# Optimization experiments

Hardware: AMD Instinct MI355X
Metric: run time of the kernel (lower is better)

Reference implementation:

```python
import jax, jax.numpy as jnp
import numpy as np

IN_C = 128
OUT_C = 128
N_NODES = 50000
N_EDGES = 500000


def setup_inputs() -> dict:
    key = jax.random.key(0)
    ks = jax.random.split(key, 12)
    s = lambda k, shp, fan: jax.random.normal(k, shp, jnp.float32) * (1.0 / np.sqrt(fan))
    return {
        "node_embeddings": jax.random.normal(ks[0], (N_NODES, IN_C), jnp.float32),
        "edge_index": jax.random.randint(ks[1], (2, N_EDGES), 0, N_NODES, jnp.int64),
        # source_proj / target_proj: Linear(in, in)
        "Ws": s(ks[2], (IN_C, IN_C), IN_C), "bs": jnp.zeros((IN_C,), jnp.float32),
        "Wt": s(ks[3], (IN_C, IN_C), IN_C), "bt": jnp.zeros((IN_C,), jnp.float32),
        # attention_mlp: Linear(2in, in) -> ReLU -> Linear(in, 1) -> Sigmoid
        "Wa1": s(ks[4], (2 * IN_C, IN_C), 2 * IN_C), "ba1": jnp.zeros((IN_C,), jnp.float32),
        "Wa2": s(ks[5], (IN_C, 1), IN_C), "ba2": jnp.zeros((1,), jnp.float32),
        # edge_mlp: Linear(2in, 2out) -> GeGLU -> LayerNorm(out)
        "We": s(ks[6], (2 * IN_C, 2 * OUT_C), 2 * IN_C), "be": jnp.zeros((2 * OUT_C,), jnp.float32),
        "gamma": jnp.ones((OUT_C,), jnp.float32), "beta": jnp.zeros((OUT_C,), jnp.float32),
    }


def reference(node_embeddings, edge_index, Ws, bs, Wt, bt, Wa1, ba1, Wa2, ba2, We, be, gamma, beta):
    # gather + dual projection  -> [E, in], [E, in]
    src = node_embeddings[edge_index[0]] @ Ws + bs
    tgt = node_embeddings[edge_index[1]] @ Wt + bt
    edge_features = jnp.concatenate([src, tgt], axis=-1)  # [E, 2*in]
    # sigmoid attention gate  -> [E, 1]
    h = jax.nn.relu(edge_features @ Wa1 + ba1)
    attn = jax.nn.sigmoid(h @ Wa2 + ba2)
    attended = edge_features * attn  # [E, 2*in]
    # edge MLP: Linear -> GeGLU -> LayerNorm
    z = attended @ We + be  # [E, 2*out]
    x, gate = jnp.split(z, 2, axis=-1)
    g = x * jax.nn.gelu(gate, approximate=False)  # [E, out]
    mu = jnp.mean(g, axis=-1, keepdims=True)
    var = jnp.var(g, axis=-1, keepdims=True)
    out = (g - mu) * jax.lax.rsqrt(var + 1e-5) * gamma + beta
    return out
```

## Files before the change

kernel.cpp:

```cpp
#include <hip/hip_runtime.h>
#include <hip/hip_bf16.h>


typedef __bf16 bf16x8 __attribute__((ext_vector_type(8)));
typedef float f32x4 __attribute__((ext_vector_type(4)));

__device__ __forceinline__ unsigned short f2b(float f) {
    unsigned int u = __float_as_uint(f);
    unsigned int r = (u + 0x7fffu + ((u >> 16) & 1u)) >> 16;
    return (unsigned short)r;
}

__device__ __forceinline__ float erf_fast(float x) {
    float ax = __builtin_fabsf(x);
    float t = __fdividef(1.f, fmaf(0.3275911f, ax, 1.f));
    float y = t * fmaf(t, fmaf(t, fmaf(t, fmaf(t, 1.061405429f, -1.453152027f),
                                       1.421413741f), -0.284496736f), 0.254829592f);
    float e = __expf(-ax * ax);
    float r = fmaf(-y, e, 1.f);
    return __builtin_copysignf(r, x);
}

__global__ __launch_bounds__(256) void pack_weights(
    const float* __restrict__ Ws, const float* __restrict__ Wt,
    const float* __restrict__ Wa1, const float* __restrict__ We,
    unsigned short* __restrict__ Wp1, unsigned short* __restrict__ Wp2)
{
    int id = blockIdx.x * 256 + threadIdx.x;
    if (id < 32768) {
        int n = id >> 7, k = id & 127;
        float v = (n < 128) ? Ws[k * 128 + n] : Wt[k * 128 + (n - 128)];
        Wp1[id] = f2b(v);
    }
    if (id < 98304) {
        int n = id >> 8, k = id & 255;
        float v = (n < 128) ? Wa1[k * 128 + n] : We[k * 256 + (n - 128)];
        Wp2[id] = f2b(v);
    }
}

__global__ __launch_bounds__(256) void node_proj(
    const float* __restrict__ emb, const unsigned short* __restrict__ Wp1,
    const float* __restrict__ bs, const float* __restrict__ bt,
    unsigned short* __restrict__ P, int NN)
{
    __shared__ __align__(16) unsigned short SH[64 * 264];
    int t = threadIdx.x;
    int base = blockIdx.x * 64;

#pragma unroll
    for (int i = 0; i < 4; ++i) {
        int c = t + i * 256;
        int row = c >> 4, cp = (c & 15) * 8;
        int node = base + row; if (node >= NN) node = NN - 1;
        const float* sp = emb + (size_t)node * 128 + cp;
        float4 v0 = *(const float4*)sp;
        float4 v1 = *(const float4*)(sp + 4);
        union { uint4 u; unsigned short s[8]; } pk;
        pk.s[0] = f2b(v0.x); pk.s[1] = f2b(v0.y); pk.s[2] = f2b(v0.z); pk.s[3] = f2b(v0.w);
        pk.s[4] = f2b(v1.x); pk.s[5] = f2b(v1.y); pk.s[6] = f2b(v1.z); pk.s[7] = f2b(v1.w);
        *(uint4*)&SH[row * 136 + cp] = pk.u;
    }
    __syncthreads();

    int wv = t >> 6, lane = t & 63, n15 = lane & 15, quad = lane >> 4;
    f32x4 z4 = {0.f, 0.f, 0.f, 0.f};
    f32x4 acc[16];
#pragma unroll
    for (int i = 0; i < 16; ++i) acc[i] = z4;

    const unsigned short* wbase = Wp1 + (size_t)(wv * 16 + n15) * 128 + quad * 8;
    for (int ks = 0; ks < 4; ++ks) {
        bf16x8 a[4];
#pragma unroll
        for (int m = 0; m < 4; ++m)
            a[m] = *(const bf16x8*)&SH[(m * 16 + n15) * 136 + ks * 32 + quad * 8];
#pragma unroll
        for (int k = 0; k < 4; ++k) {
            bf16x8 b = *(const bf16x8*)(wbase + k * 8192 + ks * 32);
#pragma unroll
            for (int m = 0; m < 4; ++m)
                acc[k * 4 + m] = __builtin_amdgcn_mfma_f32_16x16x32_bf16(a[m], b, acc[k * 4 + m], 0, 0, 0);
        }
    }
    __syncthreads();

#pragma unroll
    for (int k = 0; k < 4; ++k) {
        int colk = (wv + 4 * k) * 16 + n15;
        float bias = (colk < 128) ? bs[colk] : bt[colk - 128];
#pragma unroll
        for (int m = 0; m < 4; ++m) {
#pragma unroll
            for (int r = 0; r < 4; ++r)
                SH[(m * 16 + quad * 4 + r) * 264 + colk] = f2b(acc[k * 4 + m][r] + bias);
        }
    }
    __syncthreads();

#pragma unroll
    for (int i = 0; i < 8; ++i) {
        int e = i * 8 + (t >> 5);
        int node = base + e;
        if (node < NN) {
            int c = (t & 31) * 8;
            *(uint4*)(P + (size_t)node * 256 + c) = *(const uint4*)&SH[e * 264 + c];
        }
    }
}

__global__ __launch_bounds__(256, 3) void edge_kernel(
    const int* __restrict__ eidx, const unsigned short* __restrict__ P,
    const unsigned short* __restrict__ Wp2,
    const float* __restrict__ ba1, const float* __restrict__ Wa2,
    const float* __restrict__ ba2, const float* __restrict__ be,
    const float* __restrict__ gamma, const float* __restrict__ beta,
    float* __restrict__ out, int E)
{
    __shared__ unsigned short Alds[64][264];
    __shared__ float attnP[4][64];
    __shared__ float lnP[4][2][64];
    int t = threadIdx.x;
    int base = blockIdx.x * 64;

#pragma unroll
    for (int i = 0; i < 8; ++i) {
        int c = t + i * 256;
        int e = c >> 5, p = c & 31;
        int ge = base + e; if (ge >= E) ge = E - 1;
        int node = (p < 16) ? eidx[ge] : eidx[E + ge];
        *(uint4*)&Alds[e][p * 8] = *(const uint4*)(P + (size_t)node * 256 + p * 8);
    }
    __syncthreads();

    int wv = t >> 6, lane = t & 63, n15 = lane & 15, quad = lane >> 4;
    f32x4 z4 = {0.f, 0.f, 0.f, 0.f};
    const unsigned short* wbase = Wp2 + (size_t)(wv * 16 + n15) * 256 + quad * 8;

    f32x4 acc1[8];
#pragma unroll
    for (int i = 0; i < 8; ++i) acc1[i] = z4;
    for (int ks = 0; ks < 8; ++ks) {
        bf16x8 a[4];
#pragma unroll
        for (int m = 0; m < 4; ++m)
            a[m] = *(const bf16x8*)&Alds[m * 16 + n15][ks * 32 + quad * 8];
#pragma unroll
        for (int n = 0; n < 2; ++n) {
            bf16x8 b = *(const bf16x8*)(wbase + n * 16384 + ks * 32);
#pragma unroll
            for (int m = 0; m < 4; ++m)
                acc1[n * 4 + m] = __builtin_amdgcn_mfma_f32_16x16x32_bf16(a[m], b, acc1[n * 4 + m], 0, 0, 0);
        }
    }

    float ba2s = ba2[0];
    float ba1v[2], wa2v[2];
#pragma unroll
    for (int n = 0; n < 2; ++n) {
        int col = (wv + 4 * n) * 16 + n15;
        ba1v[n] = ba1[col]; wa2v[n] = Wa2[col];
    }
#pragma unroll
    for (int m = 0; m < 4; ++m) {
#pragma unroll
        for (int r = 0; r < 4; ++r) {
            float v = fmaxf(acc1[m][r] + ba1v[0], 0.f) * wa2v[0]
                    + fmaxf(acc1[4 + m][r] + ba1v[1], 0.f) * wa2v[1];
            v += __shfl_xor(v, 1); v += __shfl_xor(v, 2);
            v += __shfl_xor(v, 4); v += __shfl_xor(v, 8);
            if (n15 == m * 4 + r) attnP[wv][m * 16 + quad * 4 + r] = v;
        }
    }
    __syncthreads();

    float attn[4][4];
#pragma unroll
    for (int m = 0; m < 4; ++m) {
#pragma unroll
        for (int r = 0; r < 4; ++r) {
            int row = m * 16 + quad * 4 + r;
            float s = attnP[0][row] + attnP[1][row] + attnP[2][row] + attnP[3][row];
            attn[m][r] = __fdividef(1.f, 1.f + __expf(-(s + ba2s)));
        }
    }

    f32x4 acc2[16];
#pragma unroll
    for (int i = 0; i < 16; ++i) acc2[i] = z4;
    for (int ks = 0; ks < 8; ++ks) {
        bf16x8 a[4];
#pragma unroll
        for (int m = 0; m < 4; ++m)
            a[m] = *(const bf16x8*)&Alds[m * 16 + n15][ks * 32 + quad * 8];
#pragma unroll
        for (int j = 0; j < 4; ++j) {
            bf16x8 b = *(const bf16x8*)(wbase + (2 + j) * 16384 + ks * 32);
#pragma unroll
            for (int m = 0; m < 4; ++m)
                acc2[j * 4 + m] = __builtin_amdgcn_mfma_f32_16x16x32_bf16(a[m], b, acc2[j * 4 + m], 0, 0, 0);
        }
    }

    float bex[2], beg[2], gmv[2], btv[2];
#pragma unroll
    for (int j = 0; j < 2; ++j) {
        int col = wv * 16 + j * 64 + n15;
        bex[j] = be[col];       beg[j] = be[128 + col];
        gmv[j] = gamma[col];    btv[j] = beta[col];
    }
#pragma unroll
    for (int m = 0; m < 4; ++m) {
#pragma unroll
        for (int r = 0; r < 4; ++r) {
            float s1 = 0.f, s2 = 0.f;
#pragma unroll
            for (int j = 0; j < 2; ++j) {
                float zx = fmaf(attn[m][r], acc2[j * 4 + m][r], bex[j]);
                float zg = fmaf(attn[m][r], acc2[(2 + j) * 4 + m][r], beg[j]);
                float g = zx * (0.5f * zg * (1.f + erf_fast(zg * 0.70710678118f)));
                acc2[j * 4 + m][r] = g;
                s1 += g; s2 = fmaf(g, g, s2);
            }
            s1 += __shfl_xor(s1, 1); s1 += __shfl_xor(s1, 2);
            s1 += __shfl_xor(s1, 4); s1 += __shfl_xor(s1, 8);
            s2 += __shfl_xor(s2, 1); s2 += __shfl_xor(s2, 2);
            s2 += __shfl_xor(s2, 4); s2 += __shfl_xor(s2, 8);
            if (n15 == m * 4 + r) {
                lnP[wv][0][m * 16 + quad * 4 + r] = s1;
                lnP[wv][1][m * 16 + quad * 4 + r] = s2;
            }
        }
    }
    __syncthreads();

    float* Olds = (float*)Alds;
#pragma unroll
    for (int m = 0; m < 4; ++m) {
#pragma unroll
        for (int r = 0; r < 4; ++r) {
            int row = m * 16 + quad * 4 + r;
            float s1 = lnP[0][0][row] + lnP[1][0][row] + lnP[2][0][row] + lnP[3][0][row];
            float s2 = lnP[0][1][row] + lnP[1][1][row] + lnP[2][1][row] + lnP[3][1][row];
            float mu = s1 * 0.0078125f;
            float var = s2 * 0.0078125f - mu * mu;
            float rs = rsqrtf(var + 1e-5f);
            Olds[row * 132 + wv * 16 + n15]      = (acc2[m][r]     - mu) * rs * gmv[0] + btv[0];
            Olds[row * 132 + 64 + wv * 16 + n15] = (acc2[4 + m][r] - mu) * rs * gmv[1] + btv[1];
        }
    }
    __syncthreads();

#pragma unroll
    for (int i = 0; i < 8; ++i) {
        int e = i * 8 + (t >> 5);
        int edge = base + e;
        if (edge < E) {
            int c = (t & 31) * 4;
            *(float4*)(out + (size_t)edge * 128 + c) = *(const float4*)&Olds[e * 132 + c];
        }
    }
}

extern "C" void kernel_launch(void* const* d_in, const int* in_sizes, int n_in,
                              void* d_out, int out_size, void* d_ws, size_t ws_size,
                              hipStream_t stream) {
    const float* emb  = (const float*)d_in[0];
    const int*   eidx = (const int*)d_in[1];
    const float* Ws   = (const float*)d_in[2];
    const float* bs   = (const float*)d_in[3];
    const float* Wt   = (const float*)d_in[4];
    const float* bt   = (const float*)d_in[5];
    const float* Wa1  = (const float*)d_in[6];
    const float* ba1  = (const float*)d_in[7];
    const float* Wa2  = (const float*)d_in[8];
    const float* ba2  = (const float*)d_in[9];
    const float* We   = (const float*)d_in[10];
    const float* be   = (const float*)d_in[11];
    const float* gam  = (const float*)d_in[12];
    const float* bet  = (const float*)d_in[13];
    float* out = (float*)d_out;
    int NN = in_sizes[0] / 128;
    int E  = in_sizes[1] / 2;
    unsigned short* Wp1 = (unsigned short*)d_ws;
    unsigned short* Wp2 = Wp1 + 32768;
    unsigned short* P   = Wp2 + 98304;
    hipLaunchKernelGGL(pack_weights, dim3(384), dim3(256), 0, stream,
                       Ws, Wt, Wa1, We, Wp1, Wp2);
    hipLaunchKernelGGL(node_proj, dim3((NN + 63) / 64), dim3(256), 0, stream,
                       emb, Wp1, bs, bt, P, NN);
    hipLaunchKernelGGL(edge_kernel, dim3((E + 63) / 64), dim3(256), 0, stream,
                       eidx, P, Wp2, ba1, Wa2, ba2, be, gam, bet, out, E);
}
```

Measured before the change: 551.7 us.

## Prefetch weight fragments into registers and split edge GEMM into gate/value phases

Weight B-fragments are now loaded into registers before the post-gather barrier, so global weight loads overlap the LDS fill in both the projection and edge kernels. The edge MLP GEMM is split into a gate pass, whose GELU is computed right away, and a value pass with double-buffered weight prefetch, which cuts live accumulators from 16 to 8 per phase. The aim is to hide weight-load latency and ease register pressure. In exchange, the prefetch arrays add registers of their own and could lower occupancy or cause spills.

```diff
diff --git a/kernel.cpp b/kernel.cpp
--- a/kernel.cpp
+++ b/kernel.cpp
@@ -61,27 +61,35 @@
         pk.s[4] = f2b(v1.x); pk.s[5] = f2b(v1.y); pk.s[6] = f2b(v1.z); pk.s[7] = f2b(v1.w);
         *(uint4*)&SH[row * 136 + cp] = pk.u;
     }
-    __syncthreads();
 
     int wv = t >> 6, lane = t & 63, n15 = lane & 15, quad = lane >> 4;
+    const unsigned short* wbase = Wp1 + (size_t)(wv * 16 + n15) * 128 + quad * 8;
+
+    bf16x8 b[16];
+#pragma unroll
+    for (int k = 0; k < 4; ++k)
+#pragma unroll
+        for (int ks = 0; ks < 4; ++ks)
+            b[k * 4 + ks] = *(const bf16x8*)(wbase + k * 8192 + ks * 32);
+
+    __syncthreads();
+
     f32x4 z4 = {0.f, 0.f, 0.f, 0.f};
     f32x4 acc[16];
 #pragma unroll
     for (int i = 0; i < 16; ++i) acc[i] = z4;
 
-    const unsigned short* wbase = Wp1 + (size_t)(wv * 16 + n15) * 128 + quad * 8;
+#pragma unroll
     for (int ks = 0; ks < 4; ++ks) {
         bf16x8 a[4];
 #pragma unroll
         for (int m = 0; m < 4; ++m)
             a[m] = *(const bf16x8*)&SH[(m * 16 + n15) * 136 + ks * 32 + quad * 8];
 #pragma unroll
-        for (int k = 0; k < 4; ++k) {
-            bf16x8 b = *(const bf16x8*)(wbase + k * 8192 + ks * 32);
+        for (int k = 0; k < 4; ++k)
 #pragma unroll
             for (int m = 0; m < 4; ++m)
-                acc[k * 4 + m] = __builtin_amdgcn_mfma_f32_16x16x32_bf16(a[m], b, acc[k * 4 + m], 0, 0, 0);
-        }
+                acc[k * 4 + m] = __builtin_amdgcn_mfma_f32_16x16x32_bf16(a[m], b[k * 4 + ks], acc[k * 4 + m], 0, 0, 0);
     }
     __syncthreads();
 
@@ -131,27 +139,41 @@
         int node = (p < 16) ? eidx[ge] : eidx[E + ge];
         *(uint4*)&Alds[e][p * 8] = *(const uint4*)(P + (size_t)node * 256 + p * 8);
     }
-    __syncthreads();
 
     int wv = t >> 6, lane = t & 63, n15 = lane & 15, quad = lane >> 4;
+    const unsigned short* wbase = Wp2 + (size_t)(wv * 16 + n15) * 256 + quad * 8;
     f32x4 z4 = {0.f, 0.f, 0.f, 0.f};
-    const unsigned short* wbase = Wp2 + (size_t)(wv * 16 + n15) * 256 + quad * 8;
+
+    bf16x8 b1[16];
+#pragma unroll
+    for (int ks = 0; ks < 8; ++ks) {
+        b1[ks * 2]     = *(const bf16x8*)(wbase + 0 * 16384 + ks * 32);
+        b1[ks * 2 + 1] = *(const bf16x8*)(wbase + 1 * 16384 + ks * 32);
+    }
+
+    __syncthreads();
 
     f32x4 acc1[8];
 #pragma unroll
     for (int i = 0; i < 8; ++i) acc1[i] = z4;
+#pragma unroll
     for (int ks = 0; ks < 8; ++ks) {
         bf16x8 a[4];
 #pragma unroll
         for (int m = 0; m < 4; ++m)
             a[m] = *(const bf16x8*)&Alds[m * 16 + n15][ks * 32 + quad * 8];
 #pragma unroll
-        for (int n = 0; n < 2; ++n) {
-            bf16x8 b = *(const bf16x8*)(wbase + n * 16384 + ks * 32);
+        for (int n = 0; n < 2; ++n)
 #pragma unroll
             for (int m = 0; m < 4; ++m)
-                acc1[n * 4 + m] = __builtin_amdgcn_mfma_f32_16x16x32_bf16(a[m], b, acc1[n * 4 + m], 0, 0, 0);
-        }
+                acc1[n * 4 + m] = __builtin_amdgcn_mfma_f32_16x16x32_bf16(a[m], b1[ks * 2 + n], acc1[n * 4 + m], 0, 0, 0);
+    }
+
+    bf16x8 bg[16];
+#pragma unroll
+    for (int ks = 0; ks < 8; ++ks) {
+        bg[ks * 2]     = *(const bf16x8*)(wbase + 4 * 16384 + ks * 32);
+        bg[ks * 2 + 1] = *(const bf16x8*)(wbase + 5 * 16384 + ks * 32);
     }
 
     float ba2s = ba2[0];
@@ -185,21 +207,20 @@
         }
     }
 
-    f32x4 acc2[16];
-#pragma unroll
-    for (int i = 0; i < 16; ++i) acc2[i] = z4;
+    f32x4 accg[8];
+#pragma unroll
+    for (int i = 0; i < 8; ++i) accg[i] = z4;
+#pragma unroll
     for (int ks = 0; ks < 8; ++ks) {
         bf16x8 a[4];
 #pragma unroll
         for (int m = 0; m < 4; ++m)
             a[m] = *(const bf16x8*)&Alds[m * 16 + n15][ks * 32 + quad * 8];
 #pragma unroll
-        for (int j = 0; j < 4; ++j) {
-            bf16x8 b = *(const bf16x8*)(wbase + (2 + j) * 16384 + ks * 32);
+        for (int n = 0; n < 2; ++n)
 #pragma unroll
             for (int m = 0; m < 4; ++m)
-                acc2[j * 4 + m] = __builtin_amdgcn_mfma_f32_16x16x32_bf16(a[m], b, acc2[j * 4 + m], 0, 0, 0);
-        }
+                accg[n * 4 + m] = __builtin_amdgcn_mfma_f32_16x16x32_bf16(a[m], bg[ks * 2 + n], accg[n * 4 + m], 0, 0, 0);
     }
 
     float bex[2], beg[2], gmv[2], btv[2];
@@ -209,6 +230,45 @@
         bex[j] = be[col];       beg[j] = be[128 + col];
         gmv[j] = gamma[col];    btv[j] = beta[col];
     }
+    f32x4 gg[8];
+#pragma unroll
+    for (int j = 0; j < 2; ++j)
+#pragma unroll
+        for (int m = 0; m < 4; ++m)
+#pragma unroll
+            for (int r = 0; r < 4; ++r) {
+                float zg = fmaf(attn[m][r], accg[j * 4 + m][r], beg[j]);
+                gg[j * 4 + m][r] = 0.5f * zg * (1.f + erf_fast(zg * 0.70710678118f));
+            }
+
+    bf16x8 bx[8];
+#pragma unroll
+    for (int ks = 0; ks < 4; ++ks) {
+        bx[ks * 2]     = *(const bf16x8*)(wbase + 2 * 16384 + ks * 32);
+        bx[ks * 2 + 1] = *(const bf16x8*)(wbase + 3 * 16384 + ks * 32);
+    }
+    f32x4 accx[8];
+#pragma unroll
+    for (int i = 0; i < 8; ++i) accx[i] = z4;
+#pragma unroll
+    for (int ks = 0; ks < 8; ++ks) {
+        bf16x8 a[4];
+#pragma unroll
+        for (int m = 0; m < 4; ++m)
+            a[m] = *(const bf16x8*)&Alds[m * 16 + n15][ks * 32 + quad * 8];
+        bf16x8 bb0 = bx[(ks & 3) * 2], bb1 = bx[(ks & 3) * 2 + 1];
+        if (ks < 4) {
+            bx[(ks & 3) * 2]     = *(const bf16x8*)(wbase + 2 * 16384 + (ks + 4) * 32);
+            bx[(ks & 3) * 2 + 1] = *(const bf16x8*)(wbase + 3 * 16384 + (ks + 4) * 32);
+        }
+#pragma unroll
+        for (int m = 0; m < 4; ++m)
+            accx[m] = __builtin_amdgcn_mfma_f32_16x16x32_bf16(a[m], bb0, accx[m], 0, 0, 0);
+#pragma unroll
+        for (int m = 0; m < 4; ++m)
+            accx[4 + m] = __builtin_amdgcn_mfma_f32_16x16x32_bf16(a[m], bb1, accx[4 + m], 0, 0, 0);
+    }
+
 #pragma unroll
     for (int m = 0; m < 4; ++m) {
 #pragma unroll
@@ -216,10 +276,9 @@
             float s1 = 0.f, s2 = 0.f;
 #pragma unroll
             for (int j = 0; j < 2; ++j) {
-                float zx = fmaf(attn[m][r], acc2[j * 4 + m][r], bex[j]);
-                float zg = fmaf(attn[m][r], acc2[(2 + j) * 4 + m][r], beg[j]);
-                float g = zx * (0.5f * zg * (1.f + erf_fast(zg * 0.70710678118f)));
-                acc2[j * 4 + m][r] = g;
+                float zx = fmaf(attn[m][r], accx[j * 4 + m][r], bex[j]);
+                float g = zx * gg[j * 4 + m][r];
+                accx[j * 4 + m][r] = g;
                 s1 += g; s2 = fmaf(g, g, s2);
             }
             s1 += __shfl_xor(s1, 1); s1 += __shfl_xor(s1, 2);
@@ -245,8 +304,8 @@
             float mu = s1 * 0.0078125f;
             float var = s2 * 0.0078125f - mu * mu;
             float rs = rsqrtf(var + 1e-5f);
-            Olds[row * 132 + wv * 16 + n15]      = (acc2[m][r]     - mu) * rs * gmv[0] + btv[0];
-            Olds[row * 132 + 64 + wv * 16 + n15] = (acc2[4 + m][r] - mu) * rs * gmv[1] + btv[1];
+            Olds[row * 132 + wv * 16 + n15]      = (accx[m][r]     - mu) * rs * gmv[0] + btv[0];
+            Olds[row * 132 + 64 + wv * 16 + n15] = (accx[4 + m][r] - mu) * rs * gmv[1] + btv[1];
         }
     }
     __syncthreads();
```

Measured after the change: 542.9 us. No clear change (-1.6%).
